# Kernel optimization log

Hardware: AMD Instinct MI355X
Metric: run time of the kernel (lower is better)

The kernel has to match this reference:

```python
import jax, jax.numpy as jnp
import numpy as np

B, S, D, H = 8, 1024, 512, 8


def setup_inputs() -> dict:
    key = jax.random.key(0)
    ks = jax.random.split(key, 10)
    sc = 0.05
    return {
        "x": jax.random.normal(ks[0], (B, S, D), dtype=jnp.float32),
        "Wq": jax.random.normal(ks[1], (H, D, D), dtype=jnp.float32) * sc,
        "bq": jax.random.normal(ks[2], (H, D), dtype=jnp.float32) * sc,
        "Wk": jax.random.normal(ks[3], (H, D, D), dtype=jnp.float32) * sc,
        "bk": jax.random.normal(ks[4], (H, D), dtype=jnp.float32) * sc,
        "Wv": jax.random.normal(ks[5], (H, D, D), dtype=jnp.float32) * sc,
        "bv": jax.random.normal(ks[6], (H, D), dtype=jnp.float32) * sc,
        "Wo": jax.random.normal(ks[7], (H * D, D), dtype=jnp.float32) * sc,
        "bo": jax.random.normal(ks[8], (D,), dtype=jnp.float32) * sc,
    }


def reference(x, Wq, bq, Wk, bk, Wv, bv, Wo, bo):
    # Per-head full-dim projections, batched across heads.
    # x: [B,S,D]; Wq/Wk/Wv: [H,D,D]; b*: [H,D]
    q = jnp.einsum('bsd,hde->bhse', x, Wq) + bq[None, :, None, :]
    k = jnp.einsum('bsd,hde->bhse', x, Wk) + bk[None, :, None, :]
    v = jnp.einsum('bsd,hde->bhse', x, Wv) + bv[None, :, None, :]
    d = x.shape[-1]
    scores = jnp.einsum('bhse,bhte->bhst', q, k) / jnp.sqrt(jnp.float32(d))
    attn = jax.nn.softmax(scores, axis=-1)
    heads = jnp.einsum('bhst,bhte->bhse', attn, v)  # [B,H,S,D]
    # concat along feature dim (head order matches torch cat order)
    concat = jnp.transpose(heads, (0, 2, 1, 3)).reshape(x.shape[0], x.shape[1], -1)
    return concat @ Wo + bo
```

## Files before the change

### kernel.cpp

```cpp
#include <hip/hip_runtime.h>
#include <cstdint>
#include <cstddef>

#define BB 8
#define SS 1024
#define DDIM 512
#define HH 8
#define BS 8192
#define HD 4096

typedef __attribute__((ext_vector_type(4))) float f32x4;
typedef __attribute__((ext_vector_type(8))) short bf16x8;
typedef __attribute__((ext_vector_type(4))) unsigned short u16x4;


__device__ __forceinline__ unsigned short f2bf(float f) {
  union { float f; unsigned int u; } x; x.f = f;
  unsigned int r = x.u + 0x7fffu + ((x.u >> 16) & 1u);
  return (unsigned short)(r >> 16);
}

__device__ __forceinline__ void gload16(const void* g, void* l) {
  __builtin_amdgcn_global_load_lds(
      (const __attribute__((address_space(1))) unsigned int*)g,
      (__attribute__((address_space(3))) unsigned int*)l, 16, 0, 0);
}

#define BAR_LGKM() do { asm volatile("s_waitcnt lgkmcnt(0)" ::: "memory"); \
                        __builtin_amdgcn_s_barrier(); } while (0)
#define BAR_ALL()  do { asm volatile("s_waitcnt vmcnt(0) lgkmcnt(0)" ::: "memory"); \
                        __builtin_amdgcn_s_barrier(); } while (0)


__global__ void k_convert(const float* __restrict__ in, unsigned short* __restrict__ out, int n4) {
  int i = blockIdx.x * blockDim.x + threadIdx.x;
  if (i < n4) {
    float4 v = ((const float4*)in)[i];
    u16x4 o;
    o[0] = f2bf(v.x); o[1] = f2bf(v.y); o[2] = f2bf(v.z); o[3] = f2bf(v.w);
    ((u16x4*)out)[i] = o;
  }
}

__global__ void k_transpose_f2b(const float* __restrict__ in, unsigned short* __restrict__ out,
                                int R, int C) {
  __shared__ unsigned short tile[64][65];
  const int z = blockIdx.z;
  const int r0 = blockIdx.x << 6, c0 = blockIdx.y << 6;
  const float* ip = in + (size_t)z * R * C;
  unsigned short* op = out + (size_t)z * R * C;
  const int t = threadIdx.x;
#pragma unroll
  for (int i = 0; i < 16; ++i) {
    int idx = t + (i << 8); int r = idx >> 6, c = idx & 63;
    tile[r][c] = f2bf(ip[(size_t)(r0 + r) * C + (c0 + c)]);
  }
  __syncthreads();
#pragma unroll
  for (int i = 0; i < 16; ++i) {
    int idx = t + (i << 8); int c = idx >> 6, r = idx & 63;
    op[(size_t)(c0 + c) * R + (r0 + r)] = tile[r][c];
  }
}

template<int A_RS, int B_RS, int KITERS>
__device__ __forceinline__ void gemm_core(const char* Ag, const char* Bg,
                                          char* As, char* Bs, f32x4 acc[4][4]) {
  const int tid = threadIdx.x;
  const int wave = tid >> 6, lane = tid & 63;
  const int wr = (wave >> 1) << 6, wc = (wave & 1) << 6;
  const int srow = (wave << 3) + (lane >> 3);
  const int scol = ((lane & 7) << 4) ^ ((lane >> 3) << 4);

  for (int kb = 0; kb < KITERS; ++kb) {
    __syncthreads();
#pragma unroll
    for (int j = 0; j < 4; ++j) {
      gload16(Ag + (size_t)(j * 32 + srow) * A_RS + (size_t)kb * 128 + scol,
              As + j * 4096 + wave * 1024);
      gload16(Bg + (size_t)(j * 32 + srow) * B_RS + (size_t)kb * 128 + scol,
              Bs + j * 4096 + wave * 1024);
    }
    asm volatile("s_waitcnt vmcnt(0)" ::: "memory");
    __syncthreads();
#pragma unroll
    for (int ks = 0; ks < 2; ++ks) {
      bf16x8 af[4], bfr[4];
      const int kcol = (ks << 6) + ((lane >> 4) << 4);
#pragma unroll
      for (int i = 0; i < 4; ++i) {
        const int ar = wr + (i << 4) + (lane & 15);
        af[i] = *(const bf16x8*)(As + ar * 128 + (kcol ^ ((ar & 7) << 4)));
        const int br = wc + (i << 4) + (lane & 15);
        bfr[i] = *(const bf16x8*)(Bs + br * 128 + (kcol ^ ((br & 7) << 4)));
      }
#pragma unroll
      for (int i = 0; i < 4; ++i)
#pragma unroll
        for (int j = 0; j < 4; ++j)
          acc[i][j] = __builtin_amdgcn_mfma_f32_16x16x32_bf16(af[i], bfr[j], acc[i][j], 0, 0, 0);
    }
  }
}

__global__ __launch_bounds__(256, 2) void k_gemm_qkv(
    const unsigned short* __restrict__ xbf,
    const unsigned short* __restrict__ wqT, const unsigned short* __restrict__ wkT,
    const unsigned short* __restrict__ wvT,
    const float* __restrict__ bq, const float* __restrict__ bk, const float* __restrict__ bv,
    unsigned short* __restrict__ Qo, unsigned short* __restrict__ Ko,
    unsigned short* __restrict__ VTo, int b0) {
  __shared__ __align__(16) char As[16384], Bs[16384];
  const int z = blockIdx.z;
  const int p = z >> 3, h = z & 7;
  const unsigned short* wT = (p == 0) ? wqT : (p == 1) ? wkT : wvT;
  const float* bias = ((p == 0) ? bq : (p == 1) ? bk : bv) + (h << 9);
  const int m0 = blockIdx.x << 7, n0 = blockIdx.y << 7;
  const char* Ag = (const char*)xbf + ((size_t)(b0 << 10) + m0) * 1024;
  const char* Bg = (const char*)wT + (size_t)h * 524288 + (size_t)n0 * 1024;
  f32x4 acc[4][4] = {};
  gemm_core<1024, 1024, 8>(Ag, Bg, As, Bs, acc);

  const int tid = threadIdx.x, wave = tid >> 6, lane = tid & 63;
  const int wr = (wave >> 1) << 6, wc = (wave & 1) << 6;
  if (p == 2) {
#pragma unroll
    for (int j = 0; j < 4; ++j) {
      const int col = n0 + wc + (j << 4) + (lane & 15);
      const float bb = bias[col];
#pragma unroll
      for (int i = 0; i < 4; ++i) {
        const int sb = m0 + wr + (i << 4) + ((lane >> 4) << 2);
        const int lb = sb >> 10, s = sb & 1023;
        u16x4 o;
#pragma unroll
        for (int r = 0; r < 4; ++r) o[r] = f2bf(acc[i][j][r] + bb);
        *(u16x4*)(VTo + (size_t)(lb * HH + h) * 524288 +
                  (size_t)(((s >> 5) << 9) + col) * 32 + (s & 31)) = o;
      }
    }
  } else {
    unsigned short* dst = (p == 0) ? Qo : Ko;
#pragma unroll
    for (int j = 0; j < 4; ++j) {
      const int col = n0 + wc + (j << 4) + (lane & 15);
      const float bb = bias[col];
#pragma unroll
      for (int i = 0; i < 4; ++i)
#pragma unroll
        for (int r = 0; r < 4; ++r) {
          const int m = m0 + wr + (i << 4) + ((lane >> 4) << 2) + r;
          const int lb = m >> 10, s = m & 1023;
          dst[((size_t)((lb * HH + h) * SS + s) << 9) + col] = f2bf(acc[i][j][r] + bb);
        }
    }
  }
}

__global__ __launch_bounds__(256, 2) void k_gemm_out(
    const unsigned short* __restrict__ concat, const unsigned short* __restrict__ woT,
    const float* __restrict__ bo, float* __restrict__ out) {
  __shared__ __align__(16) char As[16384], Bs[16384];
  const int m0 = blockIdx.x << 7, n0 = blockIdx.y << 7;
  const char* Ag = (const char*)concat + (size_t)m0 * 8192;
  const char* Bg = (const char*)woT + (size_t)n0 * 8192;
  f32x4 acc[4][4] = {};
  gemm_core<8192, 8192, 64>(Ag, Bg, As, Bs, acc);

  const int tid = threadIdx.x, wave = tid >> 6, lane = tid & 63;
  const int wr = (wave >> 1) << 6, wc = (wave & 1) << 6;
#pragma unroll
  for (int j = 0; j < 4; ++j) {
    const int col = n0 + wc + (j << 4) + (lane & 15);
    const float bb = bo[col];
#pragma unroll
    for (int i = 0; i < 4; ++i)
#pragma unroll
      for (int r = 0; r < 4; ++r) {
        const int m = m0 + wr + (i << 4) + ((lane >> 4) << 2) + r;
        out[(size_t)m * DDIM + col] = acc[i][j][r] + bb;
      }
  }
}

__global__ __launch_bounds__(512, 1) void k_attn(
    const unsigned short* __restrict__ Qg, const unsigned short* __restrict__ Kg,
    const unsigned short* __restrict__ VT2g, unsigned short* __restrict__ Og,
    int b0) {
  __shared__ __align__(16) char smem[145408];
  float* Ssm = (float*)(smem + 131072);
  char*  Psm = smem + 139520;
  float* msm = (float*)(smem + 144640);
  float* lsm = (float*)(smem + 144896);
  float* fsm = (float*)(smem + 145152);

  const int tid = threadIdx.x, wave = tid >> 6, lane = tid & 63;
  const int bh = blockIdx.x & 15;
  const int qt = blockIdx.x >> 4;
  const int q0 = qt << 6;
  const char* Qb = (const char*)Qg + (size_t)bh * 1048576;
  const char* Kb = (const char*)Kg + (size_t)bh * 1048576;
  const char* Vb = (const char*)VT2g + (size_t)bh * 1048576;

  const int qi = wave >> 1, ni = wave & 1;
  const int l15 = lane & 15;
  const int kg16 = (lane >> 4) << 4;

  if (tid < 64) { msm[tid] = -1e30f; lsm[tid] = 0.0f; }

#define STAGE_K(KV0, BUF)                                                      \
  {                                                                            \
    _Pragma("unroll")                                                          \
    for (int j = 0; j < 4; ++j) {                                              \
      const int row = (j << 3) + wave;                                         \
      gload16(Kb + (size_t)((KV0) + row) * 1024 + ((lane << 4) ^ ((row & 7) << 4)), \
              smem + (BUF) * 32768 + row * 1024);                              \
    }                                                                          \
  }
#define STAGE_V(KT, BUF)                                                       \
  {                                                                            \
    const char* vsrc = Vb + (size_t)(KT) * 32768;                              \
    _Pragma("unroll")                                                          \
    for (int j = 0; j < 4; ++j) {                                              \
      const int idx = (j << 3) + wave;                                         \
      gload16(vsrc + idx * 1024 + (size_t)((lane >> 2) << 6) +                 \
                  ((((lane & 3) ^ ((lane >> 3) & 3))) << 4),                   \
              smem + 65536 + (BUF) * 32768 + idx * 1024);                      \
    }                                                                          \
  }

  bf16x8 qf[16];
  {
    const char* qrow = Qb + (size_t)(q0 + (qi << 4) + l15) * 1024 + kg16;
#pragma unroll
    for (int ks = 0; ks < 16; ++ks)
      qf[ks] = *(const bf16x8*)(qrow + (ks << 6));
  }
  STAGE_K(0, 0);
  STAGE_V(0, 0);

  f32x4 accO[4][4] = {};
  const float scale = 0.044194173824159216f;

  for (int kt = 0; kt < 32; ++kt) {
    const int cur = kt & 1;
    BAR_ALL();
    if (kt != 31) {
      STAGE_K((kt + 1) << 5, cur ^ 1);
      STAGE_V(kt + 1, cur ^ 1);
    }

    {
      f32x4 a0 = {}, a1 = {}, a2 = {}, a3 = {};
      const int krow = (ni << 4) + l15;
      const char* kb2 = smem + cur * 32768 + krow * 1024;
      const int ksz = (krow & 7) << 4;
      __builtin_amdgcn_s_setprio(1);
#pragma unroll
      for (int ks = 0; ks < 16; ks += 4) {
        const bf16x8 k0 = *(const bf16x8*)(kb2 + ((((ks + 0) << 6) + kg16) ^ ksz));
        const bf16x8 k1 = *(const bf16x8*)(kb2 + ((((ks + 1) << 6) + kg16) ^ ksz));
        const bf16x8 k2 = *(const bf16x8*)(kb2 + ((((ks + 2) << 6) + kg16) ^ ksz));
        const bf16x8 k3 = *(const bf16x8*)(kb2 + ((((ks + 3) << 6) + kg16) ^ ksz));
        a0 = __builtin_amdgcn_mfma_f32_16x16x32_bf16(qf[ks + 0], k0, a0, 0, 0, 0);
        a1 = __builtin_amdgcn_mfma_f32_16x16x32_bf16(qf[ks + 1], k1, a1, 0, 0, 0);
        a2 = __builtin_amdgcn_mfma_f32_16x16x32_bf16(qf[ks + 2], k2, a2, 0, 0, 0);
        a3 = __builtin_amdgcn_mfma_f32_16x16x32_bf16(qf[ks + 3], k3, a3, 0, 0, 0);
      }
      __builtin_amdgcn_s_setprio(0);
      const f32x4 s = (a0 + a1) + (a2 + a3);
      const int srow = (qi << 4) + ((lane >> 4) << 2);
      const int scol = (ni << 4) + l15;
#pragma unroll
      for (int r = 0; r < 4; ++r) Ssm[(srow + r) * 33 + scol] = s[r];
    }
    BAR_LGKM();

    {
      const int row = tid >> 3, c8 = tid & 7;
      float sv[4];
#pragma unroll
      for (int c = 0; c < 4; ++c) sv[c] = Ssm[row * 33 + (c8 << 2) + c] * scale;
      float mx = fmaxf(fmaxf(sv[0], sv[1]), fmaxf(sv[2], sv[3]));
      mx = fmaxf(mx, __shfl_xor(mx, 1));
      mx = fmaxf(mx, __shfl_xor(mx, 2));
      mx = fmaxf(mx, __shfl_xor(mx, 4));
      const float mold = msm[row];
      const float mnew = fmaxf(mold, mx);
      const float fac = __expf(mold - mnew);
      float ls = 0.0f;
      u16x4 pv;
#pragma unroll
      for (int c = 0; c < 4; ++c) {
        const float p = __expf(sv[c] - mnew);
        ls += p;
        pv[c] = f2bf(p);
      }
      ls += __shfl_xor(ls, 1);
      ls += __shfl_xor(ls, 2);
      ls += __shfl_xor(ls, 4);
      if ((tid & 7) == 0) {
        msm[row] = mnew;
        lsm[row] = lsm[row] * fac + ls;
        fsm[row] = fac;
      }
      *(u16x4*)(Psm + row * 80 + (c8 << 3)) = pv;
    }
    BAR_LGKM();

    {
      float facs[4][4];
      bf16x8 pf[4], vf[4];
      const int rb = (lane >> 4) << 2;
      const char* vb2 = smem + 65536 + cur * 32768;
      const int vswz = ((l15 >> 1) & 3) << 4;
#pragma unroll
      for (int i = 0; i < 4; ++i) {
#pragma unroll
        for (int r = 0; r < 4; ++r) facs[i][r] = fsm[(i << 4) + rb + r];
        pf[i] = *(const bf16x8*)(Psm + ((i << 4) + l15) * 80 + kg16);
      }
#pragma unroll
      for (int j = 0; j < 4; ++j) {
        const int vr = (wave << 6) + (j << 4) + l15;
        vf[j] = *(const bf16x8*)(vb2 + vr * 64 + (kg16 ^ vswz));
      }
#pragma unroll
      for (int i = 0; i < 4; ++i)
#pragma unroll
        for (int j = 0; j < 4; ++j)
#pragma unroll
          for (int r = 0; r < 4; ++r) accO[i][j][r] *= facs[i][r];
      __builtin_amdgcn_s_setprio(1);
#pragma unroll
      for (int i = 0; i < 4; ++i)
#pragma unroll
        for (int j = 0; j < 4; ++j)
          accO[i][j] = __builtin_amdgcn_mfma_f32_16x16x32_bf16(pf[i], vf[j], accO[i][j], 0, 0, 0);
      __builtin_amdgcn_s_setprio(0);
    }
  }

  {
    const int b = b0 + (bh >> 3), h = bh & 7;
    const int rb = (lane >> 4) << 2;
    float linv[4][4];
#pragma unroll
    for (int i = 0; i < 4; ++i)
#pragma unroll
      for (int r = 0; r < 4; ++r) linv[i][r] = 1.0f / lsm[(i << 4) + rb + r];
#pragma unroll
    for (int i = 0; i < 4; ++i)
#pragma unroll
      for (int j = 0; j < 4; ++j) {
        const int col = (wave << 6) + (j << 4) + l15;
#pragma unroll
        for (int r = 0; r < 4; ++r) {
          const int s = q0 + (i << 4) + rb + r;
          Og[((size_t)((b << 10) + s)) * HD + (h << 9) + col] = f2bf(accO[i][j][r] * linv[i][r]);
        }
      }
  }
#undef STAGE_K
#undef STAGE_V
}


extern "C" void kernel_launch(void* const* d_in, const int* in_sizes, int n_in,
                              void* d_out, int out_size, void* d_ws, size_t ws_size,
                              hipStream_t stream) {
  const float* x  = (const float*)d_in[0];
  const float* Wq = (const float*)d_in[1];
  const float* bq = (const float*)d_in[2];
  const float* Wk = (const float*)d_in[3];
  const float* bk = (const float*)d_in[4];
  const float* Wv = (const float*)d_in[5];
  const float* bv = (const float*)d_in[6];
  const float* Wo = (const float*)d_in[7];
  const float* bo = (const float*)d_in[8];
  float* out = (float*)d_out;
  char* ws = (char*)d_ws;

  unsigned short* xbf = (unsigned short*)(ws);
  unsigned short* wqT = (unsigned short*)(ws + 8388608);
  unsigned short* wkT = (unsigned short*)(ws + 12582912);
  unsigned short* wvT = (unsigned short*)(ws + 16777216);
  unsigned short* woT = (unsigned short*)(ws + 20971520);
  unsigned short* Cw  = (unsigned short*)(ws + 25165824);
  unsigned short* Qp  = (unsigned short*)(ws + 92274688);
  unsigned short* Kp  = (unsigned short*)(ws + 92274688 + 16777216ull);
  unsigned short* VTp = (unsigned short*)(ws + 92274688 + 2 * 16777216ull);

  k_convert<<<4096, 256, 0, stream>>>(x, xbf, BS * DDIM / 4);
  k_transpose_f2b<<<dim3(8, 8, 8), 256, 0, stream>>>(Wq, wqT, 512, 512);
  k_transpose_f2b<<<dim3(8, 8, 8), 256, 0, stream>>>(Wk, wkT, 512, 512);
  k_transpose_f2b<<<dim3(8, 8, 8), 256, 0, stream>>>(Wv, wvT, 512, 512);
  k_transpose_f2b<<<dim3(64, 8, 1), 256, 0, stream>>>(Wo, woT, 4096, 512);

  for (int b0 = 0; b0 < BB; b0 += 2) {
    k_gemm_qkv<<<dim3(16, 4, 24), 256, 0, stream>>>(xbf, wqT, wkT, wvT,
                                                    bq, bk, bv, Qp, Kp, VTp, b0);
    k_attn<<<dim3(256), 512, 0, stream>>>(Qp, Kp, VTp, Cw, b0);
  }

  k_gemm_out<<<dim3(64, 4), 256, 0, stream>>>(Cw, woT, bo, out);
}
```

Baseline: 598.1 us.

## Replace fused flash attention with separate QK GEMM, softmax, and PV GEMM kernels

Removes the fused online-softmax attention kernel. Attention now runs as three kernels per batch: a QK^T GEMM that writes fp32 scores to workspace, a row softmax that writes bf16 probabilities in place, and a PV GEMM that reuses the generic gemm_core. The batch loop goes from two batches per iteration to one, and the V layout changes to a plain transpose. This trades the barrier-heavy, low-occupancy fused loop for well-tuned GEMM tiles, at the cost of large score-matrix traffic through global memory and more kernel launches.

```diff
diff --git a/kernel.cpp b/kernel.cpp
--- a/kernel.cpp
+++ b/kernel.cpp
@@ -12,6 +12,7 @@
 typedef __attribute__((ext_vector_type(4))) float f32x4;
 typedef __attribute__((ext_vector_type(8))) short bf16x8;
 typedef __attribute__((ext_vector_type(4))) unsigned short u16x4;
+typedef __attribute__((ext_vector_type(8))) unsigned short u16x8;
 
 
 __device__ __forceinline__ unsigned short f2bf(float f) {
@@ -20,16 +21,16 @@
   return (unsigned short)(r >> 16);
 }
 
+__device__ __forceinline__ float bf2f(unsigned short u) {
+  union { unsigned int u; float f; } x; x.u = ((unsigned int)u) << 16;
+  return x.f;
+}
+
 __device__ __forceinline__ void gload16(const void* g, void* l) {
   __builtin_amdgcn_global_load_lds(
       (const __attribute__((address_space(1))) unsigned int*)g,
       (__attribute__((address_space(3))) unsigned int*)l, 16, 0, 0);
 }
-
-#define BAR_LGKM() do { asm volatile("s_waitcnt lgkmcnt(0)" ::: "memory"); \
-                        __builtin_amdgcn_s_barrier(); } while (0)
-#define BAR_ALL()  do { asm volatile("s_waitcnt vmcnt(0) lgkmcnt(0)" ::: "memory"); \
-                        __builtin_amdgcn_s_barrier(); } while (0)
 
 
 __global__ void k_convert(const float* __restrict__ in, unsigned short* __restrict__ out, int n4) {
@@ -131,12 +132,10 @@
 #pragma unroll
       for (int i = 0; i < 4; ++i) {
         const int sb = m0 + wr + (i << 4) + ((lane >> 4) << 2);
-        const int lb = sb >> 10, s = sb & 1023;
         u16x4 o;
 #pragma unroll
         for (int r = 0; r < 4; ++r) o[r] = f2bf(acc[i][j][r] + bb);
-        *(u16x4*)(VTo + (size_t)(lb * HH + h) * 524288 +
-                  (size_t)(((s >> 5) << 9) + col) * 32 + (s & 31)) = o;
+        *(u16x4*)(VTo + (size_t)h * 524288 + (size_t)col * 1024 + sb) = o;
       }
     }
   } else {
@@ -149,11 +148,94 @@
       for (int i = 0; i < 4; ++i)
 #pragma unroll
         for (int r = 0; r < 4; ++r) {
-          const int m = m0 + wr + (i << 4) + ((lane >> 4) << 2) + r;
-          const int lb = m >> 10, s = m & 1023;
-          dst[((size_t)((lb * HH + h) * SS + s) << 9) + col] = f2bf(acc[i][j][r] + bb);
+          const int s = m0 + wr + (i << 4) + ((lane >> 4) << 2) + r;
+          dst[((size_t)((h << 10) + s) << 9) + col] = f2bf(acc[i][j][r] + bb);
         }
     }
+  }
+}
+
+__global__ __launch_bounds__(256, 2) void k_gemm_s(
+    const unsigned short* __restrict__ Q, const unsigned short* __restrict__ K,
+    float* __restrict__ S) {
+  __shared__ __align__(16) char As[16384], Bs[16384];
+  const int idx = blockIdx.x;
+  const int bh = idx & 7, m0 = ((idx >> 3) & 7) << 7, n0 = (idx >> 6) << 7;
+  const char* Ag = (const char*)Q + (size_t)bh * 1048576 + (size_t)m0 * 1024;
+  const char* Bg = (const char*)K + (size_t)bh * 1048576 + (size_t)n0 * 1024;
+  f32x4 acc[4][4] = {};
+  gemm_core<1024, 1024, 8>(Ag, Bg, As, Bs, acc);
+
+  float* Sb = S + (size_t)bh * 1048576;
+  const int tid = threadIdx.x, wave = tid >> 6, lane = tid & 63;
+  const int wr = (wave >> 1) << 6, wc = (wave & 1) << 6;
+#pragma unroll
+  for (int j = 0; j < 4; ++j) {
+    const int col = n0 + wc + (j << 4) + (lane & 15);
+#pragma unroll
+    for (int i = 0; i < 4; ++i)
+#pragma unroll
+      for (int r = 0; r < 4; ++r) {
+        const int q = m0 + wr + (i << 4) + ((lane >> 4) << 2) + r;
+        Sb[(size_t)q * 1024 + col] = acc[i][j][r];
+      }
+  }
+}
+
+__global__ __launch_bounds__(256) void k_softmax(float* __restrict__ S) {
+  const int wave = threadIdx.x >> 6, lane = threadIdx.x & 63;
+  float* rp = S + ((size_t)(blockIdx.x << 2) + wave) * 1024;
+  const float scale = 0.044194173824159216f;
+  f32x4 v[4];
+#pragma unroll
+  for (int i = 0; i < 4; ++i) v[i] = ((const f32x4*)rp)[(lane << 2) + i];
+  float mx = -1e30f;
+#pragma unroll
+  for (int i = 0; i < 4; ++i)
+#pragma unroll
+    for (int c = 0; c < 4; ++c) { v[i][c] *= scale; mx = fmaxf(mx, v[i][c]); }
+#pragma unroll
+  for (int o = 1; o < 64; o <<= 1) mx = fmaxf(mx, __shfl_xor(mx, o));
+  float p[16];
+  float l = 0.0f;
+#pragma unroll
+  for (int i = 0; i < 4; ++i)
+#pragma unroll
+    for (int c = 0; c < 4; ++c) { float e = __expf(v[i][c] - mx); p[(i << 2) + c] = e; l += e; }
+#pragma unroll
+  for (int o = 1; o < 64; o <<= 1) l += __shfl_xor(l, o);
+  const float inv = 1.0f / l;
+  u16x8 o0, o1;
+#pragma unroll
+  for (int c = 0; c < 8; ++c) { o0[c] = f2bf(p[c] * inv); o1[c] = f2bf(p[8 + c] * inv); }
+  unsigned short* wp = (unsigned short*)rp + (lane << 4);
+  *(u16x8*)wp = o0;
+  *(u16x8*)(wp + 8) = o1;
+}
+
+__global__ __launch_bounds__(256, 2) void k_gemm_pv(
+    const float* __restrict__ S, const unsigned short* __restrict__ VT,
+    unsigned short* __restrict__ Og, int b0) {
+  __shared__ __align__(16) char As[16384], Bs[16384];
+  const int idx = blockIdx.x;
+  const int bh = idx & 7, n0 = ((idx >> 3) & 3) << 7, m0 = (idx >> 5) << 7;
+  const char* Ag = (const char*)S + (size_t)bh * 4194304 + (size_t)m0 * 4096;
+  const char* Bg = (const char*)VT + (size_t)bh * 1048576 + (size_t)n0 * 2048;
+  f32x4 acc[4][4] = {};
+  gemm_core<4096, 2048, 16>(Ag, Bg, As, Bs, acc);
+
+  const int tid = threadIdx.x, wave = tid >> 6, lane = tid & 63;
+  const int wr = (wave >> 1) << 6, wc = (wave & 1) << 6;
+#pragma unroll
+  for (int j = 0; j < 4; ++j) {
+    const int col = n0 + wc + (j << 4) + (lane & 15);
+#pragma unroll
+    for (int i = 0; i < 4; ++i)
+#pragma unroll
+      for (int r = 0; r < 4; ++r) {
+        const int s = m0 + wr + (i << 4) + ((lane >> 4) << 2) + r;
+        Og[((size_t)((b0 << 10) + s)) * HD + (bh << 9) + col] = f2bf(acc[i][j][r]);
+      }
   }
 }
 
@@ -181,188 +263,6 @@
         out[(size_t)m * DDIM + col] = acc[i][j][r] + bb;
       }
   }
-}
-
-__global__ __launch_bounds__(512, 1) void k_attn(
-    const unsigned short* __restrict__ Qg, const unsigned short* __restrict__ Kg,
-    const unsigned short* __restrict__ VT2g, unsigned short* __restrict__ Og,
-    int b0) {
-  __shared__ __align__(16) char smem[145408];
-  float* Ssm = (float*)(smem + 131072);
-  char*  Psm = smem + 139520;
-  float* msm = (float*)(smem + 144640);
-  float* lsm = (float*)(smem + 144896);
-  float* fsm = (float*)(smem + 145152);
-
-  const int tid = threadIdx.x, wave = tid >> 6, lane = tid & 63;
-  const int bh = blockIdx.x & 15;
-  const int qt = blockIdx.x >> 4;
-  const int q0 = qt << 6;
-  const char* Qb = (const char*)Qg + (size_t)bh * 1048576;
-  const char* Kb = (const char*)Kg + (size_t)bh * 1048576;
-  const char* Vb = (const char*)VT2g + (size_t)bh * 1048576;
-
-  const int qi = wave >> 1, ni = wave & 1;
-  const int l15 = lane & 15;
-  const int kg16 = (lane >> 4) << 4;
-
-  if (tid < 64) { msm[tid] = -1e30f; lsm[tid] = 0.0f; }
-
-#define STAGE_K(KV0, BUF)                                                      \
-  {                                                                            \
-    _Pragma("unroll")                                                          \
-    for (int j = 0; j < 4; ++j) {                                              \
-      const int row = (j << 3) + wave;                                         \
-      gload16(Kb + (size_t)((KV0) + row) * 1024 + ((lane << 4) ^ ((row & 7) << 4)), \
-              smem + (BUF) * 32768 + row * 1024);                              \
-    }                                                                          \
-  }
-#define STAGE_V(KT, BUF)                                                       \
-  {                                                                            \
-    const char* vsrc = Vb + (size_t)(KT) * 32768;                              \
-    _Pragma("unroll")                                                          \
-    for (int j = 0; j < 4; ++j) {                                              \
-      const int idx = (j << 3) + wave;                                         \
-      gload16(vsrc + idx * 1024 + (size_t)((lane >> 2) << 6) +                 \
-                  ((((lane & 3) ^ ((lane >> 3) & 3))) << 4),                   \
-              smem + 65536 + (BUF) * 32768 + idx * 1024);                      \
-    }                                                                          \
-  }
-
-  bf16x8 qf[16];
-  {
-    const char* qrow = Qb + (size_t)(q0 + (qi << 4) + l15) * 1024 + kg16;
-#pragma unroll
-    for (int ks = 0; ks < 16; ++ks)
-      qf[ks] = *(const bf16x8*)(qrow + (ks << 6));
-  }
-  STAGE_K(0, 0);
-  STAGE_V(0, 0);
-
-  f32x4 accO[4][4] = {};
-  const float scale = 0.044194173824159216f;
-
-  for (int kt = 0; kt < 32; ++kt) {
-    const int cur = kt & 1;
-    BAR_ALL();
-    if (kt != 31) {
-      STAGE_K((kt + 1) << 5, cur ^ 1);
-      STAGE_V(kt + 1, cur ^ 1);
-    }
-
-    {
-      f32x4 a0 = {}, a1 = {}, a2 = {}, a3 = {};
-      const int krow = (ni << 4) + l15;
-      const char* kb2 = smem + cur * 32768 + krow * 1024;
-      const int ksz = (krow & 7) << 4;
-      __builtin_amdgcn_s_setprio(1);
-#pragma unroll
-      for (int ks = 0; ks < 16; ks += 4) {
-        const bf16x8 k0 = *(const bf16x8*)(kb2 + ((((ks + 0) << 6) + kg16) ^ ksz));
-        const bf16x8 k1 = *(const bf16x8*)(kb2 + ((((ks + 1) << 6) + kg16) ^ ksz));
-        const bf16x8 k2 = *(const bf16x8*)(kb2 + ((((ks + 2) << 6) + kg16) ^ ksz));
-        const bf16x8 k3 = *(const bf16x8*)(kb2 + ((((ks + 3) << 6) + kg16) ^ ksz));
-        a0 = __builtin_amdgcn_mfma_f32_16x16x32_bf16(qf[ks + 0], k0, a0, 0, 0, 0);
-        a1 = __builtin_amdgcn_mfma_f32_16x16x32_bf16(qf[ks + 1], k1, a1, 0, 0, 0);
-        a2 = __builtin_amdgcn_mfma_f32_16x16x32_bf16(qf[ks + 2], k2, a2, 0, 0, 0);
-        a3 = __builtin_amdgcn_mfma_f32_16x16x32_bf16(qf[ks + 3], k3, a3, 0, 0, 0);
-      }
-      __builtin_amdgcn_s_setprio(0);
-      const f32x4 s = (a0 + a1) + (a2 + a3);
-      const int srow = (qi << 4) + ((lane >> 4) << 2);
-      const int scol = (ni << 4) + l15;
-#pragma unroll
-      for (int r = 0; r < 4; ++r) Ssm[(srow + r) * 33 + scol] = s[r];
-    }
-    BAR_LGKM();
-
-    {
-      const int row = tid >> 3, c8 = tid & 7;
-      float sv[4];
-#pragma unroll
-      for (int c = 0; c < 4; ++c) sv[c] = Ssm[row * 33 + (c8 << 2) + c] * scale;
-      float mx = fmaxf(fmaxf(sv[0], sv[1]), fmaxf(sv[2], sv[3]));
-      mx = fmaxf(mx, __shfl_xor(mx, 1));
-      mx = fmaxf(mx, __shfl_xor(mx, 2));
-      mx = fmaxf(mx, __shfl_xor(mx, 4));
-      const float mold = msm[row];
-      const float mnew = fmaxf(mold, mx);
-      const float fac = __expf(mold - mnew);
-      float ls = 0.0f;
-      u16x4 pv;
-#pragma unroll
-      for (int c = 0; c < 4; ++c) {
-        const float p = __expf(sv[c] - mnew);
-        ls += p;
-        pv[c] = f2bf(p);
-      }
-      ls += __shfl_xor(ls, 1);
-      ls += __shfl_xor(ls, 2);
-      ls += __shfl_xor(ls, 4);
-      if ((tid & 7) == 0) {
-        msm[row] = mnew;
-        lsm[row] = lsm[row] * fac + ls;
-        fsm[row] = fac;
-      }
-      *(u16x4*)(Psm + row * 80 + (c8 << 3)) = pv;
-    }
-    BAR_LGKM();
-
-    {
-      float facs[4][4];
-      bf16x8 pf[4], vf[4];
-      const int rb = (lane >> 4) << 2;
-      const char* vb2 = smem + 65536 + cur * 32768;
-      const int vswz = ((l15 >> 1) & 3) << 4;
-#pragma unroll
-      for (int i = 0; i < 4; ++i) {
-#pragma unroll
-        for (int r = 0; r < 4; ++r) facs[i][r] = fsm[(i << 4) + rb + r];
-        pf[i] = *(const bf16x8*)(Psm + ((i << 4) + l15) * 80 + kg16);
-      }
-#pragma unroll
-      for (int j = 0; j < 4; ++j) {
-        const int vr = (wave << 6) + (j << 4) + l15;
-        vf[j] = *(const bf16x8*)(vb2 + vr * 64 + (kg16 ^ vswz));
-      }
-#pragma unroll
-      for (int i = 0; i < 4; ++i)
-#pragma unroll
-        for (int j = 0; j < 4; ++j)
-#pragma unroll
-          for (int r = 0; r < 4; ++r) accO[i][j][r] *= facs[i][r];
-      __builtin_amdgcn_s_setprio(1);
-#pragma unroll
-      for (int i = 0; i < 4; ++i)
-#pragma unroll
-        for (int j = 0; j < 4; ++j)
-          accO[i][j] = __builtin_amdgcn_mfma_f32_16x16x32_bf16(pf[i], vf[j], accO[i][j], 0, 0, 0);
-      __builtin_amdgcn_s_setprio(0);
-    }
-  }
-
-  {
-    const int b = b0 + (bh >> 3), h = bh & 7;
-    const int rb = (lane >> 4) << 2;
-    float linv[4][4];
-#pragma unroll
-    for (int i = 0; i < 4; ++i)
-#pragma unroll
-      for (int r = 0; r < 4; ++r) linv[i][r] = 1.0f / lsm[(i << 4) + rb + r];
-#pragma unroll
-    for (int i = 0; i < 4; ++i)
-#pragma unroll
-      for (int j = 0; j < 4; ++j) {
-        const int col = (wave << 6) + (j << 4) + l15;
-#pragma unroll
-        for (int r = 0; r < 4; ++r) {
-          const int s = q0 + (i << 4) + rb + r;
-          Og[((size_t)((b << 10) + s)) * HD + (h << 9) + col] = f2bf(accO[i][j][r] * linv[i][r]);
-        }
-      }
-  }
-#undef STAGE_K
-#undef STAGE_V
 }
 
 
@@ -388,8 +288,9 @@
   unsigned short* woT = (unsigned short*)(ws + 20971520);
   unsigned short* Cw  = (unsigned short*)(ws + 25165824);
   unsigned short* Qp  = (unsigned short*)(ws + 92274688);
-  unsigned short* Kp  = (unsigned short*)(ws + 92274688 + 16777216ull);
-  unsigned short* VTp = (unsigned short*)(ws + 92274688 + 2 * 16777216ull);
+  unsigned short* Kp  = (unsigned short*)(ws + 100663296);
+  unsigned short* VTp = (unsigned short*)(ws + 109051904);
+  float*          Sf  = (float*)(ws + 117440512);
 
   k_convert<<<4096, 256, 0, stream>>>(x, xbf, BS * DDIM / 4);
   k_transpose_f2b<<<dim3(8, 8, 8), 256, 0, stream>>>(Wq, wqT, 512, 512);
@@ -397,10 +298,12 @@
   k_transpose_f2b<<<dim3(8, 8, 8), 256, 0, stream>>>(Wv, wvT, 512, 512);
   k_transpose_f2b<<<dim3(64, 8, 1), 256, 0, stream>>>(Wo, woT, 4096, 512);
 
-  for (int b0 = 0; b0 < BB; b0 += 2) {
-    k_gemm_qkv<<<dim3(16, 4, 24), 256, 0, stream>>>(xbf, wqT, wkT, wvT,
-                                                    bq, bk, bv, Qp, Kp, VTp, b0);
-    k_attn<<<dim3(256), 512, 0, stream>>>(Qp, Kp, VTp, Cw, b0);
+  for (int b0 = 0; b0 < BB; ++b0) {
+    k_gemm_qkv<<<dim3(8, 4, 24), 256, 0, stream>>>(xbf, wqT, wkT, wvT,
+                                                   bq, bk, bv, Qp, Kp, VTp, b0);
+    k_gemm_s<<<dim3(512), 256, 0, stream>>>(Qp, Kp, Sf);
+    k_softmax<<<dim3(2048), 256, 0, stream>>>(Sf);
+    k_gemm_pv<<<dim3(256), 256, 0, stream>>>(Sf, VTp, Cw, b0);
   }
 
   k_gemm_out<<<dim3(64, 4), 256, 0, stream>>>(Cw, woT, bo, out);
```

Result: slower. 633.7 us (+5.9%).
